# Performance work log

Hardware: AMD Instinct MI355X
Metric: run time of the kernel (lower is better)

## Reference

```python
import jax, jax.numpy as jnp
import numpy as np

N_QUBITS = 8
N_LAYERS = 3
N_FEATURES = 16
BATCH = 65536
DIM = 2 ** N_QUBITS  # 256 amplitudes
EPS = 1e-5  # torch BatchNorm1d default eps

# Precompute CNOT permutations (wire 0 = most significant bit, PennyLane order)
_idx = np.arange(DIM)
CNOT_PERMS = []
for _i in range(N_QUBITS):
    for _j in range(_i + 1, N_QUBITS):
        _c = (_idx >> (N_QUBITS - 1 - _i)) & 1
        CNOT_PERMS.append(np.where(_c == 1, _idx ^ (1 << (N_QUBITS - 1 - _j)), _idx))
# PauliZ sign table: (DIM, N_QUBITS), +1 for bit 0, -1 for bit 1
Z_SIGNS = np.stack([1.0 - 2.0 * ((_idx >> (N_QUBITS - 1 - i)) & 1) for i in range(N_QUBITS)], axis=1).astype(np.float32)


def _ry(theta):
    t = jnp.asarray(theta)
    c = jnp.cos(t / 2).astype(jnp.complex64)
    s = jnp.sin(t / 2).astype(jnp.complex64)
    return jnp.stack([jnp.stack([c, -s], -1), jnp.stack([s, c], -1)], -2)


def _rx(theta):
    t = jnp.asarray(theta)
    c = jnp.cos(t / 2).astype(jnp.complex64)
    s = (-1j) * jnp.sin(t / 2).astype(jnp.complex64)
    return jnp.stack([jnp.stack([c, s], -1), jnp.stack([s, c], -1)], -2)


def _rz(theta):
    e = jnp.exp(-0.5j * jnp.asarray(theta, jnp.complex64))
    z = jnp.zeros_like(e)
    return jnp.stack([jnp.stack([e, z], -1), jnp.stack([z, jnp.conj(e)], -1)], -2)


def _apply_1q(state, U, w):
    # state: (B, DIM); U: (2,2) shared or (B,2,2) per-sample; wire w
    B = state.shape[0]
    left, right = 2 ** w, 2 ** (N_QUBITS - 1 - w)
    s = state.reshape(B, left, 2, right)
    if U.ndim == 2:
        out = jnp.einsum('st,bpsq->bptq', U, s)
    else:
        out = jnp.einsum('bst,bpsq->bptq', U, s)
    return out.reshape(B, DIM)


def _quantum(angles, qw):
    # Batched state-vector simulation of the PennyLane circuit.
    # angles: (B, N_QUBITS) float32 encoding angles; qw: (N_LAYERS, N_QUBITS, 3)
    B = angles.shape[0]
    state = jnp.zeros((B, DIM), jnp.complex64).at[:, 0].set(1.0 + 0.0j)
    for i in range(N_QUBITS):  # RY(inputs[i]) encoding, per-sample angles
        state = _apply_1q(state, _ry(angles[:, i]), i)
    for l in range(N_LAYERS):
        for i in range(N_QUBITS):
            state = _apply_1q(state, _rx(qw[l, i, 0]), i)
            state = _apply_1q(state, _ry(qw[l, i, 1]), i)
            state = _apply_1q(state, _rz(qw[l, i, 2]), i)
        for perm in CNOT_PERMS:  # all-pairs CNOT(i, j), i < j
            state = state[:, perm]
    probs = state.real ** 2 + state.imag ** 2  # (B, DIM)
    return probs @ jnp.asarray(Z_SIGNS)  # (B, N_QUBITS) <Z_i> expectations


def _bn(h, g, b, m, v):
    # BatchNorm1d in inference mode (running stats)
    return (h - m) * jax.lax.rsqrt(v + EPS) * g + b


def _forward(x, W1, b1, g1, bt1, m1, v1, W2, b2, g2, bt2, m2, v2, W3, b3, q_weights, W4, b4, g4, bt4, m4, v4, W5, b5, W6, b6):
    h = jax.nn.relu(_bn(x @ W1.T + b1, g1, bt1, m1, v1))
    h = jax.nn.relu(_bn(h @ W2.T + b2, g2, bt2, m2, v2))
    pre = jnp.tanh(h @ W3.T + b3)  # (B, N_QUBITS)
    # Original detaches before the quantum circuit -> no grad through it
    q_out = _quantum(jax.lax.stop_gradient(pre), jax.lax.stop_gradient(q_weights))
    h = jax.nn.relu(_bn(q_out @ W4.T + b4, g4, bt4, m4, v4))
    h = jax.nn.relu(h @ W5.T + b5)
    return h @ W6.T + b6  # (B, 1)


def setup_inputs() -> dict:
    key = jax.random.key(0)
    ks = jax.random.split(key, 8)

    def lin(k, o, i):
        return (jax.random.normal(k, (o, i), jnp.float32) / np.sqrt(i)).astype(jnp.float32)

    return {
        'x': jax.random.normal(ks[0], (BATCH, N_FEATURES), jnp.float32),
        'W1': lin(ks[1], 128, N_FEATURES), 'b1': jnp.zeros((128,), jnp.float32),
        'g1': jnp.ones((128,), jnp.float32), 'bt1': jnp.zeros((128,), jnp.float32),
        'm1': jnp.zeros((128,), jnp.float32), 'v1': jnp.ones((128,), jnp.float32),
        'W2': lin(ks[2], 64, 128), 'b2': jnp.zeros((64,), jnp.float32),
        'g2': jnp.ones((64,), jnp.float32), 'bt2': jnp.zeros((64,), jnp.float32),
        'm2': jnp.zeros((64,), jnp.float32), 'v2': jnp.ones((64,), jnp.float32),
        'W3': lin(ks[3], N_QUBITS, 64), 'b3': jnp.zeros((N_QUBITS,), jnp.float32),
        'q_weights': jax.random.normal(ks[4], (N_LAYERS, N_QUBITS, 3), jnp.float32) * 0.1,
        'W4': lin(ks[5], 32, N_QUBITS), 'b4': jnp.zeros((32,), jnp.float32),
        'g4': jnp.ones((32,), jnp.float32), 'bt4': jnp.zeros((32,), jnp.float32),
        'm4': jnp.zeros((32,), jnp.float32), 'v4': jnp.ones((32,), jnp.float32),
        'W5': lin(ks[6], 16, 32), 'b5': jnp.zeros((16,), jnp.float32),
        'W6': lin(ks[7], 1, 16), 'b6': jnp.zeros((1,), jnp.float32),
    }


def reference(x, W1, b1, g1, bt1, m1, v1, W2, b2, g2, bt2, m2, v2, W3, b3, q_weights, W4, b4, g4, bt4, m4, v4, W5, b5, W6, b6):
    return _forward(x, W1, b1, g1, bt1, m1, v1, W2, b2, g2, bt2, m2, v2, W3, b3, q_weights, W4, b4, g4, bt4, m4, v4, W5, b5, W6, b6)
```

## Files before the change

kernel.cpp:

```cpp
#include <hip/hip_runtime.h>

__device__ __forceinline__ float2 cmul(float2 a, float2 b){
    return make_float2(a.x*b.x - a.y*b.y, a.x*b.y + a.y*b.x);
}
__device__ __forceinline__ float2 cadd(float2 a, float2 b){
    return make_float2(a.x + b.x, a.y + b.y);
}
__device__ __forceinline__ unsigned short f2h(float f){
    _Float16 h = (_Float16)f;
    return __builtin_bit_cast(unsigned short, h);
}

typedef _Float16 f16x8 __attribute__((ext_vector_type(8)));
typedef float    f32x4 __attribute__((ext_vector_type(4)));

__device__ __forceinline__ void split8(const float* p, f16x8& ah, f16x8& al){
    const f32x4* q = (const f32x4*)p;
    f32x4 v0 = q[0], v1 = q[1];
    float av[8] = {v0[0],v0[1],v0[2],v0[3],v1[0],v1[1],v1[2],v1[3]};
    #pragma unroll
    for (int j=0;j<8;++j){
        _Float16 h = (_Float16)av[j];
        ah[j] = h;
        al[j] = (_Float16)(av[j] - (float)h);
    }
}

__device__ __forceinline__ void build_gates(const float* qw, int l, int c, float2 (*G)[2][2]){
    if (c < 8){
        int i = c;
        float t0 = 0.5f*qw[l*24 + i*3 + 0];
        float t1 = 0.5f*qw[l*24 + i*3 + 1];
        float t2 = 0.5f*qw[l*24 + i*3 + 2];
        float c1,s1,c2,s2,c3,s3;
        sincosf(t0,&s1,&c1); sincosf(t1,&s2,&c2); sincosf(t2,&s3,&c3);
        float2 RX[2][2] = {{{c1,0.f},{0.f,-s1}},{{0.f,-s1},{c1,0.f}}};
        float2 RY[2][2] = {{{c2,0.f},{s2,0.f}},{{-s2,0.f},{c2,0.f}}};
        float2 M[2][2];
        #pragma unroll
        for (int r=0;r<2;++r)
            #pragma unroll
            for (int cc=0;cc<2;++cc)
                M[r][cc] = cadd(cmul(RY[r][0],RX[0][cc]), cmul(RY[r][1],RX[1][cc]));
        float2 e  = {c3,-s3};
        float2 ec = {c3, s3};
        G[i][0][0]=cmul(e, M[0][0]); G[i][0][1]=cmul(e, M[0][1]);
        G[i][1][0]=cmul(ec,M[1][0]); G[i][1][1]=cmul(ec,M[1][1]);
    }
}
__device__ __forceinline__ int cnot_perm(int k){
    int r = k;
    for (int i=6;i>=0;--i)
        for (int j=7;j>i;--j)
            if ((r >> (7-i)) & 1) r ^= 1 << (7-j);
    return r;
}

__global__ void k_build_prep(const float* __restrict__ qw, float2* __restrict__ U,
                       const float* __restrict__ W1, const float* __restrict__ b1,
                       const float* __restrict__ g1, const float* __restrict__ bt1,
                       const float* __restrict__ m1, const float* __restrict__ v1,
                       const float* __restrict__ W2, const float* __restrict__ b2,
                       const float* __restrict__ g2, const float* __restrict__ bt2,
                       const float* __restrict__ m2, const float* __restrict__ v2,
                       const float* __restrict__ W3,
                       unsigned short* __restrict__ H1w, float* __restrict__ c1,
                       unsigned short* __restrict__ H2w, float* __restrict__ c2,
                       unsigned short* __restrict__ H3w){
    if (blockIdx.y == 2){
        if (blockIdx.x >= 8) return;
        int tid = blockIdx.x*256 + threadIdx.x;
        const int stride = 8*256;
        for (int i=tid; i<4096; i+=stride){ int n=i>>5, k=i&31;
            float s=g1[n]*rsqrtf(v1[n]+1e-5f);
            H1w[i] = f2h(k<16 ? W1[n*16+k]*s : 0.f); }
        for (int i=tid; i<128;  i+=stride){ float s=g1[i]*rsqrtf(v1[i]+1e-5f); c1[i]=(b1[i]-m1[i])*s+bt1[i]; }
        for (int i=tid; i<8192; i+=stride){ int n=i>>7;
            float s=g2[n]*rsqrtf(v2[n]+1e-5f);
            H2w[i] = f2h(W2[i]*s); }
        for (int i=tid; i<64;   i+=stride){ float s=g2[i]*rsqrtf(v2[i]+1e-5f); c2[i]=(b2[i]-m2[i])*s+bt2[i]; }
        for (int i=tid; i<1024; i+=stride){ int n=i>>6, k=i&63;
            H3w[i] = f2h(n<8 ? W3[n*64+k] : 0.f); }
        return;
    }
    __shared__ float2 G[8][2][2];
    int l = blockIdx.y, k = blockIdx.x, c = threadIdx.x;
    build_gates(qw, l, c, G);
    __syncthreads();
    int r = cnot_perm(k);
    float2 p = {1.f, 0.f};
    #pragma unroll
    for (int i=0;i<8;++i)
        p = cmul(p, G[i][(r>>(7-i))&1][(c>>(7-i))&1]);
    U[l*65536 + k*256 + c] = p;
}

__global__ __launch_bounds__(256) void k_rowmm(const float* __restrict__ qw,
                                              const float2* __restrict__ U,
                                              unsigned short* __restrict__ WqS){
    __shared__ float2 G[8][2][2];
    __shared__ float2 vs[256];
    __shared__ float2 ws[256];
    int r = blockIdx.x, c = threadIdx.x;
    build_gates(qw, 2, c, G);
    __syncthreads();
    int pr = cnot_perm(r);
    float2 p = {1.f, 0.f};
    #pragma unroll
    for (int i=0;i<8;++i)
        p = cmul(p, G[i][(pr>>(7-i))&1][(c>>(7-i))&1]);
    vs[c] = p;
    __syncthreads();
    float2 acc = {0.f,0.f};
    #pragma unroll 8
    for (int m=0;m<256;++m)
        acc = cadd(acc, cmul(vs[m], U[65536 + m*256 + c]));
    ws[c] = acc;
    __syncthreads();
    float2 z = {0.f,0.f};
    #pragma unroll 8
    for (int m=0;m<256;++m)
        z = cadd(z, cmul(ws[m], U[m*256 + c]));
    int T = r >> 4, l15 = r & 15;
    int ks = c >> 5, lq = (c >> 3) & 3, j = c & 7;
    int lane = lq*16 + l15;
    WqS[((T     *8 + ks)*64 + lane)*8 + j] = f2h(z.x);
    WqS[(((T+16)*8 + ks)*64 + lane)*8 + j] = f2h(z.y);
}

#define A_STRIDE 264
#define P_STRIDE 269
__global__ __launch_bounds__(256,2) void k_fused(
    const float* __restrict__ x,
    const unsigned short* __restrict__ H1w, const float* __restrict__ c1,
    const unsigned short* __restrict__ H2w, const float* __restrict__ c2,
    const unsigned short* __restrict__ H3w, const float* __restrict__ b3,
    const unsigned short* __restrict__ WqS,
    const float* __restrict__ W4, const float* __restrict__ b4, const float* __restrict__ g4,
    const float* __restrict__ bt4, const float* __restrict__ m4, const float* __restrict__ v4,
    const float* __restrict__ W5, const float* __restrict__ b5,
    const float* __restrict__ W6, const float* __restrict__ b6,
    float* __restrict__ out)
{
    __shared__ __align__(16) char smem[62464];
    float* XS   = (float*)smem;
    float* H1   = (float*)(smem + 9216);
    float* H2   = (float*)(smem + 43008);
    float* preL = (float*)(smem + 60416);
    unsigned short* As = (unsigned short*)smem;
    float* probs = (float*)smem;
    float* qacc  = (float*)(smem + 34432);
    float* qout  = (float*)(smem + 42624);

    int tid = threadIdx.x;
    int row0 = blockIdx.x*64;
    int wave = tid>>6, lane = tid&63, l15 = lane&15, lq = lane>>4;
    const f32x4 zz = {0.f,0.f,0.f,0.f};

    {
        int r = tid >> 2, q = tid & 3;
        const float4* xp = (const float4*)(x + (row0 + r)*16 + q*4);
        float4 v = xp[0];
        *(float4*)(XS + r*36 + q*4) = v;
        *(float4*)(XS + r*36 + 16 + q*4) = make_float4(0.f,0.f,0.f,0.f);
    }
    __syncthreads();

    {
        f32x4 acc1[4][2];
        #pragma unroll
        for (int mt=0;mt<4;++mt){ acc1[mt][0]=zz; acc1[mt][1]=zz; }
        #pragma unroll
        for (int mt=0; mt<4; ++mt){
            f16x8 ah, al;
            split8(XS + (mt*16+l15)*36 + lq*8, ah, al);
            #pragma unroll
            for (int t=0;t<2;++t){
                int nt = wave + t*4;
                f16x8 b = *(const f16x8*)(H1w + (nt*16+l15)*32 + lq*8);
                acc1[mt][t] = __builtin_amdgcn_mfma_f32_16x16x32_f16(ah, b, acc1[mt][t], 0,0,0);
                acc1[mt][t] = __builtin_amdgcn_mfma_f32_16x16x32_f16(al, b, acc1[mt][t], 0,0,0);
            }
        }
        __syncthreads();
        #pragma unroll
        for (int t=0;t<2;++t){
            int n = (wave + t*4)*16 + l15;
            float bias = c1[n];
            #pragma unroll
            for (int mt=0; mt<4; ++mt)
                #pragma unroll
                for (int reg=0; reg<4; ++reg){
                    int rowl = mt*16 + lq*4 + reg;
                    H1[rowl*132 + n] = fmaxf(acc1[mt][t][reg] + bias, 0.f);
                }
        }
    }
    __syncthreads();

    {
        f32x4 acc2[4];
        #pragma unroll
        for (int mt=0;mt<4;++mt) acc2[mt]=zz;
        #pragma unroll
        for (int ks=0; ks<4; ++ks){
            f16x8 b = *(const f16x8*)(H2w + (wave*16+l15)*128 + ks*32 + lq*8);
            #pragma unroll
            for (int mt=0; mt<4; ++mt){
                f16x8 ah, al;
                split8(H1 + (mt*16+l15)*132 + ks*32 + lq*8, ah, al);
                acc2[mt] = __builtin_amdgcn_mfma_f32_16x16x32_f16(ah, b, acc2[mt], 0,0,0);
                acc2[mt] = __builtin_amdgcn_mfma_f32_16x16x32_f16(al, b, acc2[mt], 0,0,0);
            }
        }
        int n = wave*16 + l15;
        float bias = c2[n];
        #pragma unroll
        for (int mt=0; mt<4; ++mt)
            #pragma unroll
            for (int reg=0; reg<4; ++reg){
                int rowl = mt*16 + lq*4 + reg;
                H2[rowl*68 + n] = fmaxf(acc2[mt][reg] + bias, 0.f);
            }
    }
    __syncthreads();

    {
        f32x4 acc3 = zz;
        #pragma unroll
        for (int ks=0; ks<2; ++ks){
            f16x8 b = *(const f16x8*)(H3w + l15*64 + ks*32 + lq*8);
            f16x8 ah, al;
            split8(H2 + (wave*16+l15)*68 + ks*32 + lq*8, ah, al);
            acc3 = __builtin_amdgcn_mfma_f32_16x16x32_f16(ah, b, acc3, 0,0,0);
            acc3 = __builtin_amdgcn_mfma_f32_16x16x32_f16(al, b, acc3, 0,0,0);
        }
        if (l15 < 8){
            float bias = b3[l15];
            #pragma unroll
            for (int reg=0; reg<4; ++reg){
                int rowl = wave*16 + lq*4 + reg;
                preL[rowl*8 + l15] = tanhf(acc3[reg] + bias);
            }
        }
    }
    __syncthreads();

    {
        int row = tid & 63, q = tid >> 6;
        const float4* p4 = (const float4*)(preL + row*8);
        float4 pa = p4[0], pb = p4[1];
        float th[8] = {pa.x,pa.y,pa.z,pa.w,pb.x,pb.y,pb.z,pb.w};
        float cs[8], sn[8];
        #pragma unroll
        for (int i=0;i<8;++i){ __sincosf(0.5f*th[i], &sn[i], &cs[i]); sn[i] = -sn[i]; }
        float F = (q&2 ? sn[0] : cs[0]) * (q&1 ? sn[1] : cs[1]);
        float Pm[8], Pl[8];
        #pragma unroll
        for (int a2=0;a2<8;++a2){
            Pm[a2] = (a2&4?sn[2]:cs[2]) * (a2&2?sn[3]:cs[3]) * (a2&1?sn[4]:cs[4]);
            Pl[a2] = (a2&4?sn[5]:cs[5]) * (a2&2?sn[6]:cs[6]) * (a2&1?sn[7]:cs[7]);
        }
        __syncthreads();
        unsigned short* arow = As + row*A_STRIDE + q*64;
        #pragma unroll
        for (int mh=0;mh<8;++mh){
            float fm = F * Pm[mh];
            uint4 w;
            w.x = (unsigned)f2h(fm*Pl[0]) | ((unsigned)f2h(fm*Pl[1])<<16);
            w.y = (unsigned)f2h(fm*Pl[2]) | ((unsigned)f2h(fm*Pl[3])<<16);
            w.z = (unsigned)f2h(fm*Pl[4]) | ((unsigned)f2h(fm*Pl[5])<<16);
            w.w = (unsigned)f2h(fm*Pl[6]) | ((unsigned)f2h(fm*Pl[7])<<16);
            *reinterpret_cast<uint4*>(arow + mh*8) = w;
        }
    }
    __syncthreads();

    const f16x8* Bp[8];
    #pragma unroll
    for (int t=0;t<8;++t){
        int T = ((t>>2)<<4) + wave*4 + (t&3);
        Bp[t] = reinterpret_cast<const f16x8*>(WqS + T*4096) + lane;
    }
    const f16x8* Ap[4];
    #pragma unroll
    for (int mt=0;mt<4;++mt)
        Ap[mt] = reinterpret_cast<const f16x8*>(As + (mt*16 + l15)*A_STRIDE + lq*8);

    f32x4 acc[4][8];
    #pragma unroll
    for (int mt=0;mt<4;++mt)
        #pragma unroll
        for (int t=0;t<8;++t) acc[mt][t] = zz;

    f16x8 bfr[2][8];
    #pragma unroll
    for (int t=0;t<8;++t) bfr[0][t] = Bp[t][0];

    #pragma unroll
    for (int ks=0;ks<8;++ks){
        int cur = ks & 1;
        if (ks < 7){
            #pragma unroll
            for (int t=0;t<8;++t) bfr[cur^1][t] = Bp[t][(ks+1)*64];
        }
        f16x8 afr[4];
        #pragma unroll
        for (int mt=0;mt<4;++mt) afr[mt] = Ap[mt][ks*4];
        #pragma unroll
        for (int mt=0;mt<4;++mt)
            #pragma unroll
            for (int t=0;t<8;++t)
                acc[mt][t] = __builtin_amdgcn_mfma_f32_16x16x32_f16(afr[mt], bfr[cur][t], acc[mt][t], 0, 0, 0);
    }
    __syncthreads();

    #pragma unroll
    for (int h=0; h<2; ++h){
        #pragma unroll
        for (int mtl=0; mtl<2; ++mtl){
            int mt = h*2 + mtl;
            #pragma unroll
            for (int t=0;t<4;++t){
                #pragma unroll
                for (int reg=0;reg<4;++reg){
                    float sr = acc[mt][t][reg];
                    float si = acc[mt][t+4][reg];
                    int prow = mtl*16 + lq*4 + reg;
                    int pcol = wave*64 + t*16 + l15;
                    probs[prow*P_STRIDE + pcol] = fmaf(sr,sr,si*si);
                }
            }
        }
        __syncthreads();
        {
            int row = tid & 31, q = tid >> 5;
            const float* pb = probs + row*P_STRIDE + q*32;
            float S=0.f,z3=0.f,z4=0.f,z5=0.f,z6=0.f,z7=0.f;
            #pragma unroll
            for (int j=0;j<32;++j){
                float p = pb[j];
                S  += p;
                z3 += (j&16)? -p : p;
                z4 += (j&8) ? -p : p;
                z5 += (j&4) ? -p : p;
                z6 += (j&2) ? -p : p;
                z7 += (j&1) ? -p : p;
            }
            float* qa = qacc + (q*32 + row)*8;
            f32x4 w0 = { (q&4)? -S : S,
                         (q&2)? -S : S,
                         (q&1)? -S : S,
                         z3 };
            f32x4 w1 = { z4, z5, z6, z7 };
            *(f32x4*)qa = w0;
            *(f32x4*)(qa+4) = w1;
        }
        __syncthreads();
        {
            int r = tid >> 3, i = tid & 7;
            float v = 0.f;
            #pragma unroll
            for (int g=0; g<8; ++g) v += qacc[(g*32 + r)*8 + i];
            qout[(h*32 + r)*8 + i] = v;
        }
    }
    __syncthreads();

    if (tid < 64){
        int r = tid;
        float qv[8];
        #pragma unroll
        for (int i=0;i<8;++i) qv[i] = qout[r*8+i];
        float h4[32];
        #pragma unroll
        for (int j=0;j<32;++j){
            float a = b4[j];
            #pragma unroll
            for (int i=0;i<8;++i) a = fmaf(qv[i], W4[j*8+i], a);
            float sc = g4[j]*rsqrtf(v4[j]+1e-5f);
            a = fmaf(a - m4[j], sc, bt4[j]);
            h4[j] = fmaxf(a, 0.f);
        }
        float h5[16];
        #pragma unroll
        for (int j=0;j<16;++j){
            float a = b5[j];
            #pragma unroll
            for (int k=0;k<32;++k) a = fmaf(h4[k], W5[j*32+k], a);
            h5[j] = fmaxf(a, 0.f);
        }
        float o = b6[0];
        #pragma unroll
        for (int k=0;k<16;++k) o = fmaf(h5[k], W6[k], o);
        out[blockIdx.x*64 + r] = o;
    }
}

extern "C" void kernel_launch(void* const* d_in, const int* in_sizes, int n_in,
                              void* d_out, int out_size, void* d_ws, size_t ws_size,
                              hipStream_t stream) {
    (void)in_sizes; (void)n_in; (void)out_size; (void)ws_size;
    const float* x   = (const float*)d_in[0];
    const float* W1  = (const float*)d_in[1];
    const float* b1  = (const float*)d_in[2];
    const float* g1  = (const float*)d_in[3];
    const float* bt1 = (const float*)d_in[4];
    const float* m1  = (const float*)d_in[5];
    const float* v1  = (const float*)d_in[6];
    const float* W2  = (const float*)d_in[7];
    const float* b2  = (const float*)d_in[8];
    const float* g2  = (const float*)d_in[9];
    const float* bt2 = (const float*)d_in[10];
    const float* m2  = (const float*)d_in[11];
    const float* v2  = (const float*)d_in[12];
    const float* W3  = (const float*)d_in[13];
    const float* b3  = (const float*)d_in[14];
    const float* qw  = (const float*)d_in[15];
    const float* W4  = (const float*)d_in[16];
    const float* b4  = (const float*)d_in[17];
    const float* g4  = (const float*)d_in[18];
    const float* bt4 = (const float*)d_in[19];
    const float* m4  = (const float*)d_in[20];
    const float* v4  = (const float*)d_in[21];
    const float* W5  = (const float*)d_in[22];
    const float* b5  = (const float*)d_in[23];
    const float* W6  = (const float*)d_in[24];
    const float* b6  = (const float*)d_in[25];

    char* ws = (char*)d_ws;
    float2* U   = (float2*)ws;
    unsigned short* WqS = (unsigned short*)(U + 2*65536);
    unsigned short* H1w = WqS + 512*256;
    unsigned short* H2w = H1w + 4096;
    unsigned short* H3w = H2w + 8192;
    float* c1 = (float*)(H3w + 1024);
    float* c2 = c1 + 128;

    k_build_prep<<<dim3(256,3), 256, 0, stream>>>(qw, U,
                                  W1,b1,g1,bt1,m1,v1, W2,b2,g2,bt2,m2,v2, W3,
                                  H1w,c1,H2w,c2,H3w);
    k_rowmm<<<256, 256, 0, stream>>>(qw, U, WqS);
    k_fused<<<1024, 256, 0, stream>>>(x, H1w,c1, H2w,c2, H3w,b3, WqS,
                                      W4,b4,g4,bt4,m4,v4, W5,b5,W6,b6,
                                      (float*)d_out);
}
```

Baseline: 184.6 us.

## Store MLP activations in fp16, shrink shared memory, raise occupancy to three blocks

Hidden activations H1 and H2 are now stored in shared memory as fp16 instead of fp32. This drops the hi/lo split and halves the MFMA count for layers 2 and 3. The shared-memory buffers are rearranged to fit in about 45 KB, launch bounds go up to 3 blocks per CU, and two barriers are removed. The qacc/qout strides are padded to 9 to reduce bank conflicts. The risks are lower precision in the activations and tighter register limits.

```diff
diff --git a/kernel.cpp b/kernel.cpp
--- a/kernel.cpp
+++ b/kernel.cpp
@@ -130,7 +130,7 @@
 
 #define A_STRIDE 264
 #define P_STRIDE 269
-__global__ __launch_bounds__(256,2) void k_fused(
+__global__ __launch_bounds__(256,3) void k_fused(
     const float* __restrict__ x,
     const unsigned short* __restrict__ H1w, const float* __restrict__ c1,
     const unsigned short* __restrict__ H2w, const float* __restrict__ c2,
@@ -142,15 +142,15 @@
     const float* __restrict__ W6, const float* __restrict__ b6,
     float* __restrict__ out)
 {
-    __shared__ __align__(16) char smem[62464];
-    float* XS   = (float*)smem;
-    float* H1   = (float*)(smem + 9216);
-    float* H2   = (float*)(smem + 43008);
-    float* preL = (float*)(smem + 60416);
+    __shared__ __align__(16) char smem[45952];
+    unsigned short* H1 = (unsigned short*)smem;
+    unsigned short* H2 = (unsigned short*)(smem + 17408);
+    float* XS   = (float*)(smem + 26624);
+    float* preL = (float*)(smem + 35840);
     unsigned short* As = (unsigned short*)smem;
     float* probs = (float*)smem;
     float* qacc  = (float*)(smem + 34432);
-    float* qout  = (float*)(smem + 42624);
+    float* qout  = (float*)(smem + 43648);
 
     int tid = threadIdx.x;
     int row0 = blockIdx.x*64;
@@ -182,7 +182,6 @@
                 acc1[mt][t] = __builtin_amdgcn_mfma_f32_16x16x32_f16(al, b, acc1[mt][t], 0,0,0);
             }
         }
-        __syncthreads();
         #pragma unroll
         for (int t=0;t<2;++t){
             int n = (wave + t*4)*16 + l15;
@@ -192,7 +191,7 @@
                 #pragma unroll
                 for (int reg=0; reg<4; ++reg){
                     int rowl = mt*16 + lq*4 + reg;
-                    H1[rowl*132 + n] = fmaxf(acc1[mt][t][reg] + bias, 0.f);
+                    H1[rowl*136 + n] = f2h(fmaxf(acc1[mt][t][reg] + bias, 0.f));
                 }
         }
     }
@@ -207,10 +206,8 @@
             f16x8 b = *(const f16x8*)(H2w + (wave*16+l15)*128 + ks*32 + lq*8);
             #pragma unroll
             for (int mt=0; mt<4; ++mt){
-                f16x8 ah, al;
-                split8(H1 + (mt*16+l15)*132 + ks*32 + lq*8, ah, al);
-                acc2[mt] = __builtin_amdgcn_mfma_f32_16x16x32_f16(ah, b, acc2[mt], 0,0,0);
-                acc2[mt] = __builtin_amdgcn_mfma_f32_16x16x32_f16(al, b, acc2[mt], 0,0,0);
+                f16x8 a = *(const f16x8*)(H1 + (mt*16+l15)*136 + ks*32 + lq*8);
+                acc2[mt] = __builtin_amdgcn_mfma_f32_16x16x32_f16(a, b, acc2[mt], 0,0,0);
             }
         }
         int n = wave*16 + l15;
@@ -220,7 +217,7 @@
             #pragma unroll
             for (int reg=0; reg<4; ++reg){
                 int rowl = mt*16 + lq*4 + reg;
-                H2[rowl*68 + n] = fmaxf(acc2[mt][reg] + bias, 0.f);
+                H2[rowl*72 + n] = f2h(fmaxf(acc2[mt][reg] + bias, 0.f));
             }
     }
     __syncthreads();
@@ -230,10 +227,8 @@
         #pragma unroll
         for (int ks=0; ks<2; ++ks){
             f16x8 b = *(const f16x8*)(H3w + l15*64 + ks*32 + lq*8);
-            f16x8 ah, al;
-            split8(H2 + (wave*16+l15)*68 + ks*32 + lq*8, ah, al);
-            acc3 = __builtin_amdgcn_mfma_f32_16x16x32_f16(ah, b, acc3, 0,0,0);
-            acc3 = __builtin_amdgcn_mfma_f32_16x16x32_f16(al, b, acc3, 0,0,0);
+            f16x8 a = *(const f16x8*)(H2 + (wave*16+l15)*72 + ks*32 + lq*8);
+            acc3 = __builtin_amdgcn_mfma_f32_16x16x32_f16(a, b, acc3, 0,0,0);
         }
         if (l15 < 8){
             float bias = b3[l15];
@@ -261,7 +256,6 @@
             Pm[a2] = (a2&4?sn[2]:cs[2]) * (a2&2?sn[3]:cs[3]) * (a2&1?sn[4]:cs[4]);
             Pl[a2] = (a2&4?sn[5]:cs[5]) * (a2&2?sn[6]:cs[6]) * (a2&1?sn[7]:cs[7]);
         }
-        __syncthreads();
         unsigned short* arow = As + row*A_STRIDE + q*64;
         #pragma unroll
         for (int mh=0;mh<8;++mh){
@@ -347,22 +341,19 @@
                 z6 += (j&2) ? -p : p;
                 z7 += (j&1) ? -p : p;
             }
-            float* qa = qacc + (q*32 + row)*8;
-            f32x4 w0 = { (q&4)? -S : S,
-                         (q&2)? -S : S,
-                         (q&1)? -S : S,
-                         z3 };
-            f32x4 w1 = { z4, z5, z6, z7 };
-            *(f32x4*)qa = w0;
-            *(f32x4*)(qa+4) = w1;
+            float* qa = qacc + (q*32 + row)*9;
+            qa[0] = (q&4)? -S : S;
+            qa[1] = (q&2)? -S : S;
+            qa[2] = (q&1)? -S : S;
+            qa[3] = z3; qa[4] = z4; qa[5] = z5; qa[6] = z6; qa[7] = z7;
         }
         __syncthreads();
         {
             int r = tid >> 3, i = tid & 7;
             float v = 0.f;
             #pragma unroll
-            for (int g=0; g<8; ++g) v += qacc[(g*32 + r)*8 + i];
-            qout[(h*32 + r)*8 + i] = v;
+            for (int g=0; g<8; ++g) v += qacc[(g*32 + r)*9 + i];
+            qout[(h*32 + r)*9 + i] = v;
         }
     }
     __syncthreads();
@@ -371,7 +362,7 @@
         int r = tid;
         float qv[8];
         #pragma unroll
-        for (int i=0;i<8;++i) qv[i] = qout[r*8+i];
+        for (int i=0;i<8;++i) qv[i] = qout[r*9+i];
         float h4[32];
         #pragma unroll
         for (int j=0;j<32;++j){
```

Result: slower. 264.1 us (+43.1%).
